# Performance work log

Measured on AMD Instinct MI355X. Metric: run time of the kernel, lower is better.

The kernel has to match this reference:

```python
import jax, jax.numpy as jnp
import numpy as np

B, A, L, D, IN = 4096, 11, 8, 256, 4
HID = 64  # mlp_dim in MS_HGNN modules
LINE = 64  # line_embedding output dim


def setup_inputs() -> dict:
    key = jax.random.key(0)
    ks = jax.random.split(key, 17)
    s = 0.02
    f = jnp.float32
    return {
        "inputs": jax.random.normal(ks[0], (B * A, L, IN), f),
        "W_in": jax.random.normal(ks[1], (IN, D), f) * s,
        "b_in": jnp.zeros((D,), f),
        "W_pos": jax.random.normal(ks[2], (2 * D, D), f) * s,
        "b_pos": jnp.zeros((D,), f),
        "W_fc2": jax.random.normal(ks[3], (L * D, D), f) * s,
        "b_fc2": jnp.zeros((D,), f),
        "W_fc3": jax.random.normal(ks[4], (D + A, D), f) * s,
        "b_fc3": jnp.zeros((D,), f),
        "Wh1": jax.random.normal(ks[5], (D, HID), f) * s,
        "We1": jax.random.normal(ks[6], (2 * HID, HID), f) * s,
        "Wn1": jax.random.normal(ks[7], (HID, D), f) * s,
        "Wh2": jax.random.normal(ks[8], (D, HID), f) * s,
        "We2": jax.random.normal(ks[9], (2 * HID, HID), f) * s,
        "Wn2": jax.random.normal(ks[10], (HID, D), f) * s,
        "W_line": jax.random.normal(ks[11], (D, LINE), f) * s,
        "batch_size": B,
        "agent_num": A,
    }


def _nmp(xf, Wh, We, Wn, w=None):
    # one round of neural message passing over the (hyper)graph of agents
    h = jax.nn.relu(xf @ Wh)  # [B, A, HID]
    b, a, hd = h.shape
    hi = jnp.broadcast_to(h[:, :, None, :], (b, a, a, hd))
    hj = jnp.broadcast_to(h[:, None, :, :], (b, a, a, hd))
    e = jax.nn.relu(jnp.concatenate([hi, hj], -1) @ We)  # [B, A, A, HID]
    if w is None:
        agg = e.mean(axis=2)
    else:
        agg = (w[..., None] * e).sum(axis=2) / (w.sum(axis=2)[..., None] + 1e-6)
    return agg @ Wn  # [B, A, D]


def reference(inputs, W_in, b_in, W_pos, b_pos, W_fc2, b_fc2, W_fc3, b_fc3,
              Wh1, We1, Wn1, Wh2, We2, Wn2, W_line, batch_size, agent_num):
    d = W_in.shape[1]
    length = inputs.shape[1]
    # input_fc
    tf_in = inputs @ W_in + b_in  # [B*A, L, D]
    # positional encoding (sin/cos interleaved), concat + fc (dropout in eval)
    pos = jnp.arange(length, dtype=tf_in.dtype)[:, None]
    div = jnp.exp(jnp.arange(0, d, 2, dtype=tf_in.dtype) * (-np.log(10000.0) / d))
    ang = pos * div  # [L, D/2]
    pe = jnp.stack([jnp.sin(ang), jnp.cos(ang)], -1).reshape(length, d)
    x = jnp.concatenate([tf_in, jnp.broadcast_to(pe, tf_in.shape)], -1) @ W_pos + b_pos
    # flatten time, input_fc2
    x = x.reshape(batch_size, agent_num, length * d)
    ftraj = x @ W_fc2 + b_fc2  # [B, A, D]
    # add_category (identity one-hot per agent) + input_fc3
    eye = jnp.broadcast_to(jnp.eye(agent_num, dtype=ftraj.dtype),
                           (batch_size, agent_num, agent_num))
    ftraj = jnp.concatenate([ftraj, eye], -1) @ W_fc3 + b_fc3
    # cosine-similarity correlation + per-scene adaptive thresholding
    q = ftraj / jnp.linalg.norm(ftraj, axis=2, keepdims=True)
    corr = jnp.einsum('bad,bcd->bac', q, q)
    a = corr.min(axis=(1, 2), keepdims=True)
    thr = jnp.where(a < 0.4, 0.4,
                    jnp.where((a > 0.4) & (a < 0.6), a + 0.1, a + 0.03))
    corr = jnp.where(corr < thr, jnp.zeros_like(corr), corr)
    adj = (corr > 0).astype(ftraj.dtype)  # binarized dynamic grouping mask
    # ordinary fully-connected interaction
    ftraj_inter = _nmp(ftraj, Wh1, We1, Wn1)
    # group-masked hyper interaction + line embedding
    hyp = _nmp(ftraj, Wh2, We2, Wn2, adj)
    feat_one = hyp @ W_line  # [B, A, LINE]
    out = jnp.concatenate([ftraj, ftraj_inter, feat_one], -1)
    return out.reshape(batch_size * agent_num, -1)
```

## Files before the change

kernel.cpp:

```cpp
#include <hip/hip_runtime.h>

#define TPB 256
#define TPM 192

constexpr int B_ = 4096, A_ = 11;
constexpr int R_ = B_ * A_;

constexpr int M_O     = 0;
constexpr int M2_O    = 8192;
constexpr int WC_O    = 16384;
constexpr int XB_O    = 17408;
constexpr int CB_O    = 19456;
constexpr int B2_O    = 19712;
constexpr int WN2L_O  = 22528;
constexpr int MH1_O   = 26624;
constexpr int BH1_O   = 28672;
constexpr int MH2_O   = 29376;
constexpr int BH2_O   = 31424;
constexpr int WFA1_O  = 32768;
constexpr int WFA2_O  = 49152;
constexpr int BEYE1_O = 65536;
constexpr int BEYE2_O = 66240;
constexpr int BB1_O   = 66944;
constexpr int BB2_O   = 67008;
constexpr int AG1_O   = 67584;
constexpr int SZ_RH   = R_ * 64;
constexpr int AG2_O   = AG1_O + SZ_RH;


__global__ __launch_bounds__(TPB) void k_preA(const float* __restrict__ Win,
                                              const float* __restrict__ bin,
                                              const float* __restrict__ Wpos,
                                              const float* __restrict__ bpos,
                                              const float* __restrict__ Wn2,
                                              const float* __restrict__ Wline,
                                              const float* __restrict__ Wfc3,
                                              const float* __restrict__ bfc3,
                                              const float* __restrict__ Wh1,
                                              const float* __restrict__ Wh2,
                                              float* __restrict__ ws) {
    __shared__ float red[8 * 33];
    const int t = threadIdx.x, o8 = t & 31, ks = t >> 5;
    const int bx = blockIdx.x;
    float p = 0.f;
    float base_add = 0.f;
    int out_idx = -1;
    if (bx < 64) {
        int o = bx * 32 + o8, l = o >> 8, j = o & 255;
        const float c0 = -logf(10000.f) / 256.f;
        for (int d = ks * 64; d < ks * 64 + 64; ++d) {
            float a;
            if (d < 256) a = bin[d];
            else {
                int dd = d - 256;
                float freq = expf((float)(dd & ~1) * c0);
                float ang = (float)l * freq;
                a = (dd & 1) ? cosf(ang) : sinf(ang);
            }
            p += a * Wpos[d * 256 + j];
        }
        out_idx = XB_O + o; base_add = bpos[j];
    } else if (bx < 192) {
        int o = (bx - 64) * 32 + o8, k = o >> 6, c = o & 63;
        #pragma unroll 8
        for (int d = ks * 32; d < ks * 32 + 32; ++d) p += Wn2[k * 256 + d] * Wline[d * 64 + c];
        out_idx = WN2L_O + o;
    } else if (bx < 704) {
        int o = (bx - 192) * 32 + o8, e = o >> 6, c = o & 63;
        #pragma unroll 8
        for (int d = ks * 32; d < ks * 32 + 32; ++d) p += Wfc3[e * 256 + d] * Wh1[d * 64 + c];
        out_idx = WFA1_O + o;
    } else if (bx < 1216) {
        int o = (bx - 704) * 32 + o8, e = o >> 6, c = o & 63;
        #pragma unroll 8
        for (int d = ks * 32; d < ks * 32 + 32; ++d) p += Wfc3[e * 256 + d] * Wh2[d * 64 + c];
        out_idx = WFA2_O + o;
    } else if (bx < 1238) {
        int o = (bx - 1216) * 32 + o8, a = o >> 6, c = o & 63;
        #pragma unroll 8
        for (int d = ks * 32; d < ks * 32 + 32; ++d) p += Wfc3[(256 + a) * 256 + d] * Wh1[d * 64 + c];
        out_idx = BEYE1_O + o;
    } else if (bx < 1260) {
        int o = (bx - 1238) * 32 + o8, a = o >> 6, c = o & 63;
        #pragma unroll 8
        for (int d = ks * 32; d < ks * 32 + 32; ++d) p += Wfc3[(256 + a) * 256 + d] * Wh2[d * 64 + c];
        out_idx = BEYE2_O + o;
    } else if (bx < 1262) {
        int c = (bx - 1260) * 32 + o8;
        #pragma unroll 8
        for (int d = ks * 32; d < ks * 32 + 32; ++d) p += bfc3[d] * Wh1[d * 64 + c];
        out_idx = BB1_O + c;
    } else if (bx < 1264) {
        int c = (bx - 1262) * 32 + o8;
        #pragma unroll 8
        for (int d = ks * 32; d < ks * 32 + 32; ++d) p += bfc3[d] * Wh2[d * 64 + c];
        out_idx = BB2_O + c;
    } else {
        int o = (bx - 1264) * 32 + o8, i = o >> 8, j = o & 255;
        #pragma unroll 8
        for (int d = ks * 32; d < ks * 32 + 32; ++d) p += Win[i * 256 + d] * Wpos[d * 256 + j];
        out_idx = WC_O + o;
    }
    red[ks * 33 + o8] = p;
    __shared__ float baseS[32];
    if (ks == 0) baseS[o8] = base_add;
    __syncthreads();
    if (t < 32) {
        float s = baseS[t];
        #pragma unroll
        for (int m = 0; m < 8; ++m) s += red[m * 33 + t];
        ws[out_idx - o8 + t] = s;
    }
}

__global__ __launch_bounds__(TPB) void k_preC(const float* __restrict__ Wfc2,
                                              const float* __restrict__ bfc2,
                                              float* __restrict__ ws) {
    __shared__ float red[8 * 33];
    const int t = threadIdx.x, o8 = t & 31, ks = t >> 5;
    const int bx = blockIdx.x;
    if (bx < 256) {
        int o = bx * 32 + o8, k = o >> 8, j = o & 255;
        int l = k >> 2, i = k & 3;
        const float* Ar = ws + WC_O + i * 256;
        const float* Br = Wfc2 + l * 65536 + j;
        float p = 0.f;
        #pragma unroll 8
        for (int d = ks * 32; d < ks * 32 + 32; ++d) p += Ar[d] * Br[d * 256];
        red[ks * 33 + o8] = p;
        __syncthreads();
        if (t < 32) {
            float s = 0.f;
            #pragma unroll
            for (int m = 0; m < 8; ++m) s += red[m * 33 + t];
            ws[M_O + bx * 32 + t] = s;
        }
    } else {
        int j = (bx - 256) * 32 + o8;
        const float* Ar = ws + XB_O;
        float p = 0.f;
        #pragma unroll 4
        for (int dk = ks * 256; dk < ks * 256 + 256; ++dk) p += Ar[dk] * Wfc2[dk * 256 + j];
        red[ks * 33 + o8] = p;
        __syncthreads();
        if (t < 32) {
            int jj = (bx - 256) * 32 + t;
            float s = bfc2[jj];
            #pragma unroll
            for (int m = 0; m < 8; ++m) s += red[m * 33 + t];
            ws[CB_O + jj] = s;
        }
    }
}

__global__ __launch_bounds__(TPB) void k_preD(const float* __restrict__ Wfc3,
                                              const float* __restrict__ bfc3,
                                              float* __restrict__ ws) {
    __shared__ float red[8 * 33];
    const int t = threadIdx.x, o8 = t & 31, ks = t >> 5;
    const int bx = blockIdx.x;
    float p = 0.f;
    int out_base = -1;
    int oo32 = 0;
    if (bx < 256) {
        int o = bx * 32 + o8, k = o >> 8, j = o & 255;
        const float* Ar = ws + M_O + k * 256;
        #pragma unroll 8
        for (int d = ks * 32; d < ks * 32 + 32; ++d) p += Ar[d] * Wfc3[d * 256 + j];
        out_base = M2_O; oo32 = bx * 32;
    } else if (bx < 344) {
        int o = (bx - 256) * 32 + o8, j = o & 255;
        const float* Ar = ws + CB_O;
        #pragma unroll 8
        for (int d = ks * 32; d < ks * 32 + 32; ++d) p += Ar[d] * Wfc3[d * 256 + j];
        out_base = B2_O; oo32 = (bx - 256) * 32;
    } else if (bx < 408) {
        int o = (bx - 344) * 32 + o8, k = o >> 6, c = o & 63;
        const float* Ar = ws + M_O + k * 256;
        const float* Br = ws + WFA1_O;
        #pragma unroll 8
        for (int d = ks * 32; d < ks * 32 + 32; ++d) p += Ar[d] * Br[d * 64 + c];
        out_base = MH1_O; oo32 = (bx - 344) * 32;
    } else if (bx < 472) {
        int o = (bx - 408) * 32 + o8, k = o >> 6, c = o & 63;
        const float* Ar = ws + M_O + k * 256;
        const float* Br = ws + WFA2_O;
        #pragma unroll 8
        for (int d = ks * 32; d < ks * 32 + 32; ++d) p += Ar[d] * Br[d * 64 + c];
        out_base = MH2_O; oo32 = (bx - 408) * 32;
    } else if (bx < 494) {
        int o = (bx - 472) * 32 + o8, c = o & 63;
        const float* Ar = ws + CB_O;
        const float* Br = ws + WFA1_O;
        #pragma unroll 8
        for (int d = ks * 32; d < ks * 32 + 32; ++d) p += Ar[d] * Br[d * 64 + c];
        out_base = BH1_O; oo32 = (bx - 472) * 32;
    } else {
        int o = (bx - 494) * 32 + o8, c = o & 63;
        const float* Ar = ws + CB_O;
        const float* Br = ws + WFA2_O;
        #pragma unroll 8
        for (int d = ks * 32; d < ks * 32 + 32; ++d) p += Ar[d] * Br[d * 64 + c];
        out_base = BH2_O; oo32 = (bx - 494) * 32;
    }
    red[ks * 33 + o8] = p;
    __syncthreads();
    if (t < 32) {
        int oo = oo32 + t;
        float s;
        if (out_base == B2_O) {
            int aa = oo >> 8, jj = oo & 255;
            s = bfc3[jj] + Wfc3[(256 + aa) * 256 + jj];
        } else if (out_base == BH1_O) {
            int aa = oo >> 6, cc = oo & 63;
            s = ws[BB1_O + cc] + ws[BEYE1_O + aa * 64 + cc];
        } else if (out_base == BH2_O) {
            int aa = oo >> 6, cc = oo & 63;
            s = ws[BB2_O + cc] + ws[BEYE2_O + aa * 64 + cc];
        } else s = 0.f;
        #pragma unroll
        for (int m = 0; m < 8; ++m) s += red[m * 33 + t];
        ws[out_base + oo] = s;
    }
}


__global__ __launch_bounds__(TPM) void k_main(const float* __restrict__ in,
                                              const float* __restrict__ We1g,
                                              const float* __restrict__ We2g,
                                              float* ws,
                                              float* out) {
    __shared__ float inS[22 * 36];
    __shared__ float buf[22 * 68];
    __shared__ float Bs[2048];
    __shared__ float dcS[242];
    __shared__ float thrS[2];
    const int t = threadIdx.x;
    const int rg = t >> 4, cg = t & 15;
    const int r0 = rg * 2, c0 = cg * 4;
    const int rowBlk = blockIdx.x * 22;
    const bool act = rg < 11;

    float4 pf0, pf1, pf2;
    auto pfLoad = [&](const float4* lo, const float4* hi) {
        pf0 = lo[t];
        pf1 = (t < 64) ? lo[t + 192] : hi[t - 64];
        if (t < 128) pf2 = hi[t + 128];
    };
    auto pfStore = [&]() {
        float4* d = (float4*)Bs;
        d[t] = pf0; d[t + 192] = pf1;
        if (t < 128) d[t + 384] = pf2;
    };

    pfLoad((const float4*)(ws + M2_O), (const float4*)(ws + M2_O) + 256);
    for (int o = t; o < 176; o += TPM) {
        int row = o >> 3, c4 = o & 7;
        *(float4*)&inS[row * 36 + c4 * 4] =
            *(const float4*)&in[(size_t)(rowBlk + row) * 32 + c4 * 4];
    }
    __syncthreads();

    float acc[2][16];
    #pragma unroll
    for (int r = 0; r < 2; ++r)
        #pragma unroll
        for (int c = 0; c < 16; ++c) acc[r][c] = 0.f;
    for (int kh = 0; kh < 4; ++kh) {
        pfStore();
        if (kh < 3) pfLoad((const float4*)(ws + M2_O) + (kh + 1) * 512,
                           (const float4*)(ws + M2_O) + (kh + 1) * 512 + 256);
        else        pfLoad((const float4*)(ws + MH1_O), (const float4*)(ws + MH1_O) + 256);
        __syncthreads();
        if (act) {
            #pragma unroll
            for (int kq = 0; kq < 2; ++kq) {
                float av[2][4];
                #pragma unroll
                for (int r = 0; r < 2; ++r) {
                    float4 a4 = *(const float4*)&inS[(r0 + r) * 36 + kh * 8 + kq * 4];
                    av[r][0] = a4.x; av[r][1] = a4.y; av[r][2] = a4.z; av[r][3] = a4.w;
                }
                #pragma unroll
                for (int kk = 0; kk < 4; ++kk) {
                    float4 b[4];
                    #pragma unroll
                    for (int j = 0; j < 4; ++j)
                        b[j] = *(const float4*)&Bs[(kq * 4 + kk) * 256 + c0 + j * 64];
                    #pragma unroll
                    for (int r = 0; r < 2; ++r) {
                        float a = av[r][kk];
                        #pragma unroll
                        for (int j = 0; j < 4; ++j) {
                            acc[r][j * 4 + 0] += a * b[j].x;
                            acc[r][j * 4 + 1] += a * b[j].y;
                            acc[r][j * 4 + 2] += a * b[j].z;
                            acc[r][j * 4 + 3] += a * b[j].w;
                        }
                    }
                }
            }
        }
        __syncthreads();
    }
    if (act) {
        #pragma unroll
        for (int r = 0; r < 2; ++r) {
            int row = r0 + r, il = row % 11;
            size_t ob = (size_t)(rowBlk + row) * 576;
            #pragma unroll
            for (int j = 0; j < 4; ++j) {
                float4 b2 = *(const float4*)&ws[B2_O + il * 256 + c0 + j * 64];
                acc[r][j * 4 + 0] += b2.x; acc[r][j * 4 + 1] += b2.y;
                acc[r][j * 4 + 2] += b2.z; acc[r][j * 4 + 3] += b2.w;
                *(float4*)&out[ob + c0 + j * 64] =
                    make_float4(acc[r][j * 4 + 0], acc[r][j * 4 + 1],
                                acc[r][j * 4 + 2], acc[r][j * 4 + 3]);
            }
        }
    }

    bool has0 = false;
    int s0_ = 0, i0_ = 0, j0_ = 0;
    if (t < 132) {
        has0 = true; s0_ = t / 66; int p = t % 66; int i = 0;
        while (p >= 11 - i) { p -= 11 - i; ++i; }
        i0_ = i; j0_ = i + p;
    }
    float dacc0 = 0.f;
    #pragma unroll
    for (int sl = 0; sl < 4; ++sl) {
        if (act) {
            #pragma unroll
            for (int r = 0; r < 2; ++r)
                *(float4*)&buf[(r0 + r) * 68 + c0] =
                    make_float4(acc[r][sl * 4 + 0], acc[r][sl * 4 + 1],
                                acc[r][sl * 4 + 2], acc[r][sl * 4 + 3]);
        }
        __syncthreads();
        if (has0) {
            const float* ra = &buf[(s0_ * 11 + i0_) * 68];
            const float* rb = &buf[(s0_ * 11 + j0_) * 68];
            #pragma unroll
            for (int c = 0; c < 16; ++c) {
                float4 a = *(const float4*)&ra[c * 4];
                float4 b = *(const float4*)&rb[c * 4];
                dacc0 += a.x * b.x + a.y * b.y + a.z * b.z + a.w * b.w;
            }
        }
        __syncthreads();
    }
    if (has0) { dcS[s0_ * 121 + i0_ * 11 + j0_] = dacc0;
                dcS[s0_ * 121 + j0_ * 11 + i0_] = dacc0; }
    __syncthreads();

    {
        float cc0, cc1 = 0.f;
        {
            int idx = t; int si = idx / 121, p = idx % 121, i = p / 11, j = p % 11;
            cc0 = dcS[idx] * rsqrtf(dcS[si * 121 + i * 12] * dcS[si * 121 + j * 12]);
        }
        if (t + TPM < 242) {
            int idx = t + TPM; int si = idx / 121, p = idx % 121, i = p / 11, j = p % 11;
            cc1 = dcS[idx] * rsqrtf(dcS[si * 121 + i * 12] * dcS[si * 121 + j * 12]);
        }
        __syncthreads();
        dcS[t] = cc0;
        if (t + TPM < 242) dcS[t + TPM] = cc1;
    }
    __syncthreads();
    if (t < 2) {
        float mn = 3.0e38f;
        for (int p = 0; p < 121; ++p) mn = fminf(mn, dcS[t * 121 + p]);
        thrS[t] = (mn < 0.4f) ? 0.4f : ((mn > 0.4f && mn < 0.6f) ? mn + 0.1f : mn + 0.03f);
    }
    __syncthreads();

    for (int st = 0; st < 2; ++st) {
        const float* bh = ws + (st ? BH2_O : BH1_O);
        const float* We = st ? We2g : We1g;
        pfStore();
        pfLoad((const float4*)(We), (const float4*)(We + 4096));
        __syncthreads();
        float hh[2][4];
        #pragma unroll
        for (int r = 0; r < 2; ++r)
            #pragma unroll
            for (int c = 0; c < 4; ++c) hh[r][c] = 0.f;
        if (act) {
            #pragma unroll
            for (int kq = 0; kq < 8; ++kq) {
                float av[2][4];
                #pragma unroll
                for (int r = 0; r < 2; ++r) {
                    float4 a4 = *(const float4*)&inS[(r0 + r) * 36 + kq * 4];
                    av[r][0] = a4.x; av[r][1] = a4.y; av[r][2] = a4.z; av[r][3] = a4.w;
                }
                #pragma unroll
                for (int kk = 0; kk < 4; ++kk) {
                    float4 b = *(const float4*)&Bs[(kq * 4 + kk) * 64 + c0];
                    #pragma unroll
                    for (int r = 0; r < 2; ++r) {
                        float a = av[r][kk];
                        hh[r][0] += a * b.x; hh[r][1] += a * b.y;
                        hh[r][2] += a * b.z; hh[r][3] += a * b.w;
                    }
                }
            }
            #pragma unroll
            for (int r = 0; r < 2; ++r) {
                int il = (r0 + r) % 11;
                float4 b = *(const float4*)&bh[il * 64 + c0];
                *(float4*)&buf[(r0 + r) * 68 + c0] =
                    make_float4(fmaxf(hh[r][0] + b.x, 0.f), fmaxf(hh[r][1] + b.y, 0.f),
                                fmaxf(hh[r][2] + b.z, 0.f), fmaxf(hh[r][3] + b.w, 0.f));
            }
        }
        __syncthreads();
        float uu[2][4], vv[2][4];
        #pragma unroll
        for (int r = 0; r < 2; ++r)
            #pragma unroll
            for (int c = 0; c < 4; ++c) { uu[r][c] = 0.f; vv[r][c] = 0.f; }
        for (int kh = 0; kh < 4; ++kh) {
            pfStore();
            if (kh < 3)
                pfLoad((const float4*)(We + (kh + 1) * 1024),
                       (const float4*)(We + 4096 + (kh + 1) * 1024));
            else if (st == 0)
                pfLoad((const float4*)(ws + MH2_O), (const float4*)(ws + MH2_O) + 256);
            __syncthreads();
            if (act) {
                #pragma unroll
                for (int kq = 0; kq < 4; ++kq) {
                    float av[2][4];
                    #pragma unroll
                    for (int r = 0; r < 2; ++r) {
                        float4 a4 = *(const float4*)&buf[(r0 + r) * 68 + kh * 16 + kq * 4];
                        av[r][0] = a4.x; av[r][1] = a4.y; av[r][2] = a4.z; av[r][3] = a4.w;
                    }
                    #pragma unroll
                    for (int kk = 0; kk < 4; ++kk) {
                        float4 bu = *(const float4*)&Bs[(kq * 4 + kk) * 64 + c0];
                        float4 bv = *(const float4*)&Bs[1024 + (kq * 4 + kk) * 64 + c0];
                        #pragma unroll
                        for (int r = 0; r < 2; ++r) {
                            float a = av[r][kk];
                            uu[r][0] += a * bu.x; uu[r][1] += a * bu.y;
                            uu[r][2] += a * bu.z; uu[r][3] += a * bu.w;
                            vv[r][0] += a * bv.x; vv[r][1] += a * bv.y;
                            vv[r][2] += a * bv.z; vv[r][3] += a * bv.w;
                        }
                    }
                }
            }
            __syncthreads();
        }
        if (act) {
            #pragma unroll
            for (int r = 0; r < 2; ++r)
                *(float4*)&buf[(r0 + r) * 68 + c0] =
                    make_float4(vv[r][0], vv[r][1], vv[r][2], vv[r][3]);
        }
        __syncthreads();
        if (act) {
            float* ag = ws + (st ? AG2_O : AG1_O);
            #pragma unroll
            for (int r = 0; r < 2; ++r) {
                int row = r0 + r, s = row / 11, il = row - s * 11;
                float th = thrS[s];
                float t0 = 0.f, t1 = 0.f, t2 = 0.f, t3 = 0.f, cnt = 0.f;
                #pragma unroll
                for (int j = 0; j < 11; ++j) {
                    float4 vj = *(const float4*)&buf[(s * 11 + j) * 68 + c0];
                    if (st == 0) {
                        t0 += fmaxf(uu[r][0] + vj.x, 0.f);
                        t1 += fmaxf(uu[r][1] + vj.y, 0.f);
                        t2 += fmaxf(uu[r][2] + vj.z, 0.f);
                        t3 += fmaxf(uu[r][3] + vj.w, 0.f);
                    } else {
                        float adj = (dcS[s * 121 + il * 11 + j] >= th) ? 1.f : 0.f;
                        t0 += adj * fmaxf(uu[r][0] + vj.x, 0.f);
                        t1 += adj * fmaxf(uu[r][1] + vj.y, 0.f);
                        t2 += adj * fmaxf(uu[r][2] + vj.z, 0.f);
                        t3 += adj * fmaxf(uu[r][3] + vj.w, 0.f);
                        cnt += adj;
                    }
                }
                float inv = (st == 0) ? (1.f / 11.f) : (1.f / (cnt + 1e-6f));
                *(float4*)&ag[(size_t)(rowBlk + row) * 64 + c0] =
                    make_float4(t0 * inv, t1 * inv, t2 * inv, t3 * inv);
            }
        }
        __syncthreads();
    }
}


__global__ __launch_bounds__(TPB) void k_tail(const float* __restrict__ Wn1,
                                              const float* __restrict__ ws,
                                              float* __restrict__ out) {
    __shared__ float aS[32 * 68];
    __shared__ float Bs[2048];
    const int t = threadIdx.x;
    const int rowBase = blockIdx.x * 32;
    const int tg = t >> 4, tc = t & 15;
    const int r0 = tg * 2, c0 = tc * 4;

    float4 pf0, pf1;
    auto pfLoad = [&](const float* src) {
        const float4* s = (const float4*)src;
        pf0 = s[t]; pf1 = s[t + 256];
    };
    auto pfStore = [&]() {
        float4* d = (float4*)Bs;
        d[t] = pf0; d[t + 256] = pf1;
    };

    pfLoad(Wn1);
    {
        const float4* s1 = (const float4*)(ws + AG1_O + (size_t)rowBase * 64);
        #pragma unroll
        for (int o = t; o < 512; o += TPB) {
            int row = o >> 4, c4 = o & 15;
            *(float4*)&aS[row * 68 + c4 * 4] = s1[o];
        }
    }

    float acc[2][16];
    #pragma unroll
    for (int r = 0; r < 2; ++r)
        #pragma unroll
        for (int c = 0; c < 16; ++c) acc[r][c] = 0.f;
    for (int kh = 0; kh < 8; ++kh) {
        pfStore();
        pfLoad(kh < 7 ? Wn1 + (kh + 1) * 2048 : ws + WN2L_O);
        __syncthreads();
        #pragma unroll
        for (int kq = 0; kq < 2; ++kq) {
            float av[2][4];
            #pragma unroll
            for (int r = 0; r < 2; ++r) {
                float4 a4 = *(const float4*)&aS[(r0 + r) * 68 + kh * 8 + kq * 4];
                av[r][0] = a4.x; av[r][1] = a4.y; av[r][2] = a4.z; av[r][3] = a4.w;
            }
            #pragma unroll
            for (int kk = 0; kk < 4; ++kk) {
                float4 b[4];
                #pragma unroll
                for (int j = 0; j < 4; ++j)
                    b[j] = *(const float4*)&Bs[(kq * 4 + kk) * 256 + c0 + j * 64];
                #pragma unroll
                for (int r = 0; r < 2; ++r) {
                    float a = av[r][kk];
                    #pragma unroll
                    for (int j = 0; j < 4; ++j) {
                        acc[r][j * 4 + 0] += a * b[j].x;
                        acc[r][j * 4 + 1] += a * b[j].y;
                        acc[r][j * 4 + 2] += a * b[j].z;
                        acc[r][j * 4 + 3] += a * b[j].w;
                    }
                }
            }
        }
        __syncthreads();
    }
    #pragma unroll
    for (int r = 0; r < 2; ++r) {
        size_t ob = (size_t)(rowBase + r0 + r) * 576 + 256;
        #pragma unroll
        for (int j = 0; j < 4; ++j)
            *(float4*)&out[ob + c0 + j * 64] =
                make_float4(acc[r][j * 4 + 0], acc[r][j * 4 + 1],
                            acc[r][j * 4 + 2], acc[r][j * 4 + 3]);
    }

    pfStore();
    pfLoad(ws + WN2L_O + 2048);
    {
        const float4* s2 = (const float4*)(ws + AG2_O + (size_t)rowBase * 64);
        #pragma unroll
        for (int o = t; o < 512; o += TPB) {
            int row = o >> 4, c4 = o & 15;
            *(float4*)&aS[row * 68 + c4 * 4] = s2[o];
        }
    }
    float fa[2][4];
    #pragma unroll
    for (int r = 0; r < 2; ++r)
        #pragma unroll
        for (int c = 0; c < 4; ++c) fa[r][c] = 0.f;
    for (int kh = 0; kh < 2; ++kh) {
        __syncthreads();
        if (kh == 1) { pfStore(); __syncthreads(); }
        #pragma unroll
        for (int kq = 0; kq < 8; ++kq) {
            float av[2][4];
            #pragma unroll
            for (int r = 0; r < 2; ++r) {
                float4 a4 = *(const float4*)&aS[(r0 + r) * 68 + kh * 32 + kq * 4];
                av[r][0] = a4.x; av[r][1] = a4.y; av[r][2] = a4.z; av[r][3] = a4.w;
            }
            #pragma unroll
            for (int kk = 0; kk < 4; ++kk) {
                float4 b = *(const float4*)&Bs[(kq * 4 + kk) * 64 + c0];
                #pragma unroll
                for (int r = 0; r < 2; ++r) {
                    float a = av[r][kk];
                    fa[r][0] += a * b.x; fa[r][1] += a * b.y;
                    fa[r][2] += a * b.z; fa[r][3] += a * b.w;
                }
            }
        }
    }
    #pragma unroll
    for (int r = 0; r < 2; ++r)
        *(float4*)&out[(size_t)(rowBase + r0 + r) * 576 + 512 + c0] =
            make_float4(fa[r][0], fa[r][1], fa[r][2], fa[r][3]);
}

extern "C" void kernel_launch(void* const* d_in, const int* in_sizes, int n_in,
                              void* d_out, int out_size, void* d_ws, size_t ws_size,
                              hipStream_t stream) {
    (void)in_sizes; (void)n_in; (void)out_size; (void)ws_size;
    const float* in     = (const float*)d_in[0];
    const float* W_in   = (const float*)d_in[1];
    const float* b_in   = (const float*)d_in[2];
    const float* W_pos  = (const float*)d_in[3];
    const float* b_pos  = (const float*)d_in[4];
    const float* W_fc2  = (const float*)d_in[5];
    const float* b_fc2  = (const float*)d_in[6];
    const float* W_fc3  = (const float*)d_in[7];
    const float* b_fc3  = (const float*)d_in[8];
    const float* Wh1    = (const float*)d_in[9];
    const float* We1    = (const float*)d_in[10];
    const float* Wn1    = (const float*)d_in[11];
    const float* Wh2    = (const float*)d_in[12];
    const float* We2    = (const float*)d_in[13];
    const float* Wn2    = (const float*)d_in[14];
    const float* W_line = (const float*)d_in[15];
    float* out = (float*)d_out;
    float* ws  = (float*)d_ws;

    k_preA<<<1296, TPB, 0, stream>>>(W_in, b_in, W_pos, b_pos, Wn2, W_line,
                                     W_fc3, b_fc3, Wh1, Wh2, ws);
    k_preC<<<264, TPB, 0, stream>>>(W_fc2, b_fc2, ws);
    k_preD<<<516, TPB, 0, stream>>>(W_fc3, b_fc3, ws);
    k_main<<<R_ / 22, TPM, 0, stream>>>(in, We1, We2, ws, out);
    k_tail<<<R_ / 32, TPB, 0, stream>>>(Wn1, ws, out);
}
```

Before: 154.8 us.

## Fuse tail projection GEMMs into main kernel, drop aggregate workspace round-trip

The separate k_tail kernel is removed. Its two projections (agg1 @ Wn1 into columns 256..511 and agg2 @ Wn2·W_line into columns 512..575) now run inside k_main, reading the aggregated messages from shared memory instead of writing them to workspace and reloading them. This removes one kernel launch and about 2×45K×64 floats of global write-plus-read traffic. In exchange, k_main gets more registers per thread and extra synchronisation phases, and only 176 of its 192 threads do useful work in the new GEMMs.

```diff
diff --git a/kernel.cpp b/kernel.cpp
--- a/kernel.cpp
+++ b/kernel.cpp
@@ -23,9 +23,6 @@
 constexpr int BEYE2_O = 66240;
 constexpr int BB1_O   = 66944;
 constexpr int BB2_O   = 67008;
-constexpr int AG1_O   = 67584;
-constexpr int SZ_RH   = R_ * 64;
-constexpr int AG2_O   = AG1_O + SZ_RH;
 
 
 __global__ __launch_bounds__(TPB) void k_preA(const float* __restrict__ Win,
@@ -228,8 +225,9 @@
 __global__ __launch_bounds__(TPM) void k_main(const float* __restrict__ in,
                                               const float* __restrict__ We1g,
                                               const float* __restrict__ We2g,
-                                              float* ws,
-                                              float* out) {
+                                              const float* __restrict__ Wn1,
+                                              const float* __restrict__ ws,
+                                              float* __restrict__ out) {
     __shared__ float inS[22 * 36];
     __shared__ float buf[22 * 68];
     __shared__ float Bs[2048];
@@ -428,7 +426,9 @@
                 pfLoad((const float4*)(We + (kh + 1) * 1024),
                        (const float4*)(We + 4096 + (kh + 1) * 1024));
             else if (st == 0)
-                pfLoad((const float4*)(ws + MH2_O), (const float4*)(ws + MH2_O) + 256);
+                pfLoad((const float4*)(Wn1), (const float4*)(Wn1) + 256);
+            else
+                pfLoad((const float4*)(ws + WN2L_O), (const float4*)(ws + WN2L_O) + 256);
             __syncthreads();
             if (act) {
                 #pragma unroll
@@ -463,8 +463,8 @@
                     make_float4(vv[r][0], vv[r][1], vv[r][2], vv[r][3]);
         }
         __syncthreads();
+        float ag[2][4];
         if (act) {
-            float* ag = ws + (st ? AG2_O : AG1_O);
             #pragma unroll
             for (int r = 0; r < 2; ++r) {
                 int row = r0 + r, s = row / 11, il = row - s * 11;
@@ -488,135 +488,115 @@
                     }
                 }
                 float inv = (st == 0) ? (1.f / 11.f) : (1.f / (cnt + 1e-6f));
-                *(float4*)&ag[(size_t)(rowBlk + row) * 64 + c0] =
-                    make_float4(t0 * inv, t1 * inv, t2 * inv, t3 * inv);
-            }
-        }
-        __syncthreads();
-    }
-}
-
-
-__global__ __launch_bounds__(TPB) void k_tail(const float* __restrict__ Wn1,
-                                              const float* __restrict__ ws,
-                                              float* __restrict__ out) {
-    __shared__ float aS[32 * 68];
-    __shared__ float Bs[2048];
-    const int t = threadIdx.x;
-    const int rowBase = blockIdx.x * 32;
-    const int tg = t >> 4, tc = t & 15;
-    const int r0 = tg * 2, c0 = tc * 4;
-
-    float4 pf0, pf1;
-    auto pfLoad = [&](const float* src) {
-        const float4* s = (const float4*)src;
-        pf0 = s[t]; pf1 = s[t + 256];
-    };
-    auto pfStore = [&]() {
-        float4* d = (float4*)Bs;
-        d[t] = pf0; d[t + 256] = pf1;
-    };
-
-    pfLoad(Wn1);
-    {
-        const float4* s1 = (const float4*)(ws + AG1_O + (size_t)rowBase * 64);
-        #pragma unroll
-        for (int o = t; o < 512; o += TPB) {
-            int row = o >> 4, c4 = o & 15;
-            *(float4*)&aS[row * 68 + c4 * 4] = s1[o];
-        }
-    }
-
-    float acc[2][16];
-    #pragma unroll
-    for (int r = 0; r < 2; ++r)
-        #pragma unroll
-        for (int c = 0; c < 16; ++c) acc[r][c] = 0.f;
-    for (int kh = 0; kh < 8; ++kh) {
-        pfStore();
-        pfLoad(kh < 7 ? Wn1 + (kh + 1) * 2048 : ws + WN2L_O);
-        __syncthreads();
-        #pragma unroll
-        for (int kq = 0; kq < 2; ++kq) {
-            float av[2][4];
-            #pragma unroll
-            for (int r = 0; r < 2; ++r) {
-                float4 a4 = *(const float4*)&aS[(r0 + r) * 68 + kh * 8 + kq * 4];
-                av[r][0] = a4.x; av[r][1] = a4.y; av[r][2] = a4.z; av[r][3] = a4.w;
-            }
-            #pragma unroll
-            for (int kk = 0; kk < 4; ++kk) {
-                float4 b[4];
-                #pragma unroll
-                for (int j = 0; j < 4; ++j)
-                    b[j] = *(const float4*)&Bs[(kq * 4 + kk) * 256 + c0 + j * 64];
+                ag[r][0] = t0 * inv; ag[r][1] = t1 * inv;
+                ag[r][2] = t2 * inv; ag[r][3] = t3 * inv;
+            }
+        }
+        __syncthreads();
+        if (act) {
+            #pragma unroll
+            for (int r = 0; r < 2; ++r)
+                *(float4*)&buf[(r0 + r) * 68 + c0] =
+                    make_float4(ag[r][0], ag[r][1], ag[r][2], ag[r][3]);
+        }
+        __syncthreads();
+
+        if (st == 0) {
+            float ac2[2][16];
+            #pragma unroll
+            for (int r = 0; r < 2; ++r)
+                #pragma unroll
+                for (int c = 0; c < 16; ++c) ac2[r][c] = 0.f;
+            for (int kh = 0; kh < 8; ++kh) {
+                pfStore();
+                if (kh < 7) pfLoad((const float4*)(Wn1) + (kh + 1) * 512,
+                                   (const float4*)(Wn1) + (kh + 1) * 512 + 256);
+                else        pfLoad((const float4*)(ws + MH2_O), (const float4*)(ws + MH2_O) + 256);
+                __syncthreads();
+                if (act) {
+                    #pragma unroll
+                    for (int kq = 0; kq < 2; ++kq) {
+                        float av[2][4];
+                        #pragma unroll
+                        for (int r = 0; r < 2; ++r) {
+                            float4 a4 = *(const float4*)&buf[(r0 + r) * 68 + kh * 8 + kq * 4];
+                            av[r][0] = a4.x; av[r][1] = a4.y; av[r][2] = a4.z; av[r][3] = a4.w;
+                        }
+                        #pragma unroll
+                        for (int kk = 0; kk < 4; ++kk) {
+                            float4 b[4];
+                            #pragma unroll
+                            for (int j = 0; j < 4; ++j)
+                                b[j] = *(const float4*)&Bs[(kq * 4 + kk) * 256 + c0 + j * 64];
+                            #pragma unroll
+                            for (int r = 0; r < 2; ++r) {
+                                float a = av[r][kk];
+                                #pragma unroll
+                                for (int j = 0; j < 4; ++j) {
+                                    ac2[r][j * 4 + 0] += a * b[j].x;
+                                    ac2[r][j * 4 + 1] += a * b[j].y;
+                                    ac2[r][j * 4 + 2] += a * b[j].z;
+                                    ac2[r][j * 4 + 3] += a * b[j].w;
+                                }
+                            }
+                        }
+                    }
+                }
+                __syncthreads();
+            }
+            if (act) {
                 #pragma unroll
                 for (int r = 0; r < 2; ++r) {
-                    float a = av[r][kk];
-                    #pragma unroll
-                    for (int j = 0; j < 4; ++j) {
-                        acc[r][j * 4 + 0] += a * b[j].x;
-                        acc[r][j * 4 + 1] += a * b[j].y;
-                        acc[r][j * 4 + 2] += a * b[j].z;
-                        acc[r][j * 4 + 3] += a * b[j].w;
+                    size_t ob = (size_t)(rowBlk + r0 + r) * 576 + 256;
+                    #pragma unroll
+                    for (int j = 0; j < 4; ++j)
+                        *(float4*)&out[ob + c0 + j * 64] =
+                            make_float4(ac2[r][j * 4 + 0], ac2[r][j * 4 + 1],
+                                        ac2[r][j * 4 + 2], ac2[r][j * 4 + 3]);
+                }
+            }
+        } else {
+            float fa[2][4];
+            #pragma unroll
+            for (int r = 0; r < 2; ++r)
+                #pragma unroll
+                for (int c = 0; c < 4; ++c) fa[r][c] = 0.f;
+            for (int kh = 0; kh < 2; ++kh) {
+                pfStore();
+                if (kh == 0) pfLoad((const float4*)(ws + WN2L_O) + 512,
+                                    (const float4*)(ws + WN2L_O) + 768);
+                __syncthreads();
+                if (act) {
+                    #pragma unroll
+                    for (int kq = 0; kq < 8; ++kq) {
+                        float av[2][4];
+                        #pragma unroll
+                        for (int r = 0; r < 2; ++r) {
+                            float4 a4 = *(const float4*)&buf[(r0 + r) * 68 + kh * 32 + kq * 4];
+                            av[r][0] = a4.x; av[r][1] = a4.y; av[r][2] = a4.z; av[r][3] = a4.w;
+                        }
+                        #pragma unroll
+                        for (int kk = 0; kk < 4; ++kk) {
+                            float4 b = *(const float4*)&Bs[(kq * 4 + kk) * 64 + c0];
+                            #pragma unroll
+                            for (int r = 0; r < 2; ++r) {
+                                float a = av[r][kk];
+                                fa[r][0] += a * b.x; fa[r][1] += a * b.y;
+                                fa[r][2] += a * b.z; fa[r][3] += a * b.w;
+                            }
+                        }
                     }
                 }
-            }
-        }
-        __syncthreads();
-    }
-    #pragma unroll
-    for (int r = 0; r < 2; ++r) {
-        size_t ob = (size_t)(rowBase + r0 + r) * 576 + 256;
-        #pragma unroll
-        for (int j = 0; j < 4; ++j)
-            *(float4*)&out[ob + c0 + j * 64] =
-                make_float4(acc[r][j * 4 + 0], acc[r][j * 4 + 1],
-                            acc[r][j * 4 + 2], acc[r][j * 4 + 3]);
-    }
-
-    pfStore();
-    pfLoad(ws + WN2L_O + 2048);
-    {
-        const float4* s2 = (const float4*)(ws + AG2_O + (size_t)rowBase * 64);
-        #pragma unroll
-        for (int o = t; o < 512; o += TPB) {
-            int row = o >> 4, c4 = o & 15;
-            *(float4*)&aS[row * 68 + c4 * 4] = s2[o];
-        }
-    }
-    float fa[2][4];
-    #pragma unroll
-    for (int r = 0; r < 2; ++r)
-        #pragma unroll
-        for (int c = 0; c < 4; ++c) fa[r][c] = 0.f;
-    for (int kh = 0; kh < 2; ++kh) {
-        __syncthreads();
-        if (kh == 1) { pfStore(); __syncthreads(); }
-        #pragma unroll
-        for (int kq = 0; kq < 8; ++kq) {
-            float av[2][4];
-            #pragma unroll
-            for (int r = 0; r < 2; ++r) {
-                float4 a4 = *(const float4*)&aS[(r0 + r) * 68 + kh * 32 + kq * 4];
-                av[r][0] = a4.x; av[r][1] = a4.y; av[r][2] = a4.z; av[r][3] = a4.w;
-            }
-            #pragma unroll
-            for (int kk = 0; kk < 4; ++kk) {
-                float4 b = *(const float4*)&Bs[(kq * 4 + kk) * 64 + c0];
-                #pragma unroll
-                for (int r = 0; r < 2; ++r) {
-                    float a = av[r][kk];
-                    fa[r][0] += a * b.x; fa[r][1] += a * b.y;
-                    fa[r][2] += a * b.z; fa[r][3] += a * b.w;
-                }
-            }
-        }
-    }
-    #pragma unroll
-    for (int r = 0; r < 2; ++r)
-        *(float4*)&out[(size_t)(rowBase + r0 + r) * 576 + 512 + c0] =
-            make_float4(fa[r][0], fa[r][1], fa[r][2], fa[r][3]);
+                if (kh == 0) __syncthreads();
+            }
+            if (act) {
+                #pragma unroll
+                for (int r = 0; r < 2; ++r)
+                    *(float4*)&out[(size_t)(rowBlk + r0 + r) * 576 + 512 + c0] =
+                        make_float4(fa[r][0], fa[r][1], fa[r][2], fa[r][3]);
+            }
+        }
+    }
 }
 
 extern "C" void kernel_launch(void* const* d_in, const int* in_sizes, int n_in,
@@ -646,6 +626,5 @@
                                      W_fc3, b_fc3, Wh1, Wh2, ws);
     k_preC<<<264, TPB, 0, stream>>>(W_fc2, b_fc2, ws);
     k_preD<<<516, TPB, 0, stream>>>(W_fc3, b_fc3, ws);
-    k_main<<<R_ / 22, TPM, 0, stream>>>(in, We1, We2, ws, out);
-    k_tail<<<R_ / 32, TPB, 0, stream>>>(Wn1, ws, out);
+    k_main<<<R_ / 22, TPM, 0, stream>>>(in, We1, We2, Wn1, ws, out);
 }
```

New measurement: 186.1 us. +20.2%, slower.

## Process one scene per block in k_main instead of two

Applied to the files above, without the earlier changes.

k_main now handles a single scene (11 agent rows) per block with one row per thread group, and launches 4096 blocks instead of 2048. Per-thread register tiles shrink from 2 rows to 1, shared-memory footprint drops, and the correlation/threshold logic is simplified to one scene. This trades register-level reuse of each shared-memory weight load (now used for one row instead of two) for more blocks, lower register pressure and higher occupancy. Weight staging is also repeated across twice as many blocks, which adds global and shared traffic.

```diff
diff --git a/kernel.cpp b/kernel.cpp
--- a/kernel.cpp
+++ b/kernel.cpp
@@ -230,15 +230,16 @@
                                               const float* __restrict__ We2g,
                                               float* ws,
                                               float* out) {
-    __shared__ float inS[22 * 36];
-    __shared__ float buf[22 * 68];
+    __shared__ float inS[11 * 36];
+    __shared__ float buf[11 * 68];
     __shared__ float Bs[2048];
-    __shared__ float dcS[242];
-    __shared__ float thrS[2];
+    __shared__ float dcS[121];
+    __shared__ float thrS1;
     const int t = threadIdx.x;
     const int rg = t >> 4, cg = t & 15;
-    const int r0 = rg * 2, c0 = cg * 4;
-    const int rowBlk = blockIdx.x * 22;
+    const int c0 = cg * 4;
+    const int row = rg;
+    const int rowBlk = blockIdx.x * 11;
     const bool act = rg < 11;
 
     float4 pf0, pf1, pf2;
@@ -254,18 +255,16 @@
     };
 
     pfLoad((const float4*)(ws + M2_O), (const float4*)(ws + M2_O) + 256);
-    for (int o = t; o < 176; o += TPM) {
-        int row = o >> 3, c4 = o & 7;
-        *(float4*)&inS[row * 36 + c4 * 4] =
-            *(const float4*)&in[(size_t)(rowBlk + row) * 32 + c4 * 4];
+    if (t < 88) {
+        int r = t >> 3, c4 = t & 7;
+        *(float4*)&inS[r * 36 + c4 * 4] =
+            *(const float4*)&in[(size_t)(rowBlk + r) * 32 + c4 * 4];
     }
     __syncthreads();
 
-    float acc[2][16];
+    float acc[16];
     #pragma unroll
-    for (int r = 0; r < 2; ++r)
-        #pragma unroll
-        for (int c = 0; c < 16; ++c) acc[r][c] = 0.f;
+    for (int c = 0; c < 16; ++c) acc[c] = 0.f;
     for (int kh = 0; kh < 4; ++kh) {
         pfStore();
         if (kh < 3) pfLoad((const float4*)(ws + M2_O) + (kh + 1) * 512,
@@ -275,28 +274,21 @@
         if (act) {
             #pragma unroll
             for (int kq = 0; kq < 2; ++kq) {
-                float av[2][4];
-                #pragma unroll
-                for (int r = 0; r < 2; ++r) {
-                    float4 a4 = *(const float4*)&inS[(r0 + r) * 36 + kh * 8 + kq * 4];
-                    av[r][0] = a4.x; av[r][1] = a4.y; av[r][2] = a4.z; av[r][3] = a4.w;
-                }
+                float4 a4 = *(const float4*)&inS[row * 36 + kh * 8 + kq * 4];
+                float av[4] = {a4.x, a4.y, a4.z, a4.w};
                 #pragma unroll
                 for (int kk = 0; kk < 4; ++kk) {
                     float4 b[4];
                     #pragma unroll
                     for (int j = 0; j < 4; ++j)
                         b[j] = *(const float4*)&Bs[(kq * 4 + kk) * 256 + c0 + j * 64];
+                    float a = av[kk];
                     #pragma unroll
-                    for (int r = 0; r < 2; ++r) {
-                        float a = av[r][kk];
-                        #pragma unroll
-                        for (int j = 0; j < 4; ++j) {
-                            acc[r][j * 4 + 0] += a * b[j].x;
-                            acc[r][j * 4 + 1] += a * b[j].y;
-                            acc[r][j * 4 + 2] += a * b[j].z;
-                            acc[r][j * 4 + 3] += a * b[j].w;
-                        }
+                    for (int j = 0; j < 4; ++j) {
+                        acc[j * 4 + 0] += a * b[j].x;
+                        acc[j * 4 + 1] += a * b[j].y;
+                        acc[j * 4 + 2] += a * b[j].z;
+                        acc[j * 4 + 3] += a * b[j].w;
                     }
                 }
             }
@@ -304,43 +296,36 @@
         __syncthreads();
     }
     if (act) {
-        #pragma unroll
-        for (int r = 0; r < 2; ++r) {
-            int row = r0 + r, il = row % 11;
-            size_t ob = (size_t)(rowBlk + row) * 576;
-            #pragma unroll
-            for (int j = 0; j < 4; ++j) {
-                float4 b2 = *(const float4*)&ws[B2_O + il * 256 + c0 + j * 64];
-                acc[r][j * 4 + 0] += b2.x; acc[r][j * 4 + 1] += b2.y;
-                acc[r][j * 4 + 2] += b2.z; acc[r][j * 4 + 3] += b2.w;
-                *(float4*)&out[ob + c0 + j * 64] =
-                    make_float4(acc[r][j * 4 + 0], acc[r][j * 4 + 1],
-                                acc[r][j * 4 + 2], acc[r][j * 4 + 3]);
-            }
+        size_t ob = (size_t)(rowBlk + row) * 576;
+        #pragma unroll
+        for (int j = 0; j < 4; ++j) {
+            float4 b2 = *(const float4*)&ws[B2_O + row * 256 + c0 + j * 64];
+            acc[j * 4 + 0] += b2.x; acc[j * 4 + 1] += b2.y;
+            acc[j * 4 + 2] += b2.z; acc[j * 4 + 3] += b2.w;
+            *(float4*)&out[ob + c0 + j * 64] =
+                make_float4(acc[j * 4 + 0], acc[j * 4 + 1],
+                            acc[j * 4 + 2], acc[j * 4 + 3]);
         }
     }
 
     bool has0 = false;
-    int s0_ = 0, i0_ = 0, j0_ = 0;
-    if (t < 132) {
-        has0 = true; s0_ = t / 66; int p = t % 66; int i = 0;
+    int i0_ = 0, j0_ = 0;
+    if (t < 66) {
+        has0 = true; int p = t; int i = 0;
         while (p >= 11 - i) { p -= 11 - i; ++i; }
         i0_ = i; j0_ = i + p;
     }
     float dacc0 = 0.f;
     #pragma unroll
     for (int sl = 0; sl < 4; ++sl) {
-        if (act) {
-            #pragma unroll
-            for (int r = 0; r < 2; ++r)
-                *(float4*)&buf[(r0 + r) * 68 + c0] =
-                    make_float4(acc[r][sl * 4 + 0], acc[r][sl * 4 + 1],
-                                acc[r][sl * 4 + 2], acc[r][sl * 4 + 3]);
-        }
+        if (act)
+            *(float4*)&buf[row * 68 + c0] =
+                make_float4(acc[sl * 4 + 0], acc[sl * 4 + 1],
+                            acc[sl * 4 + 2], acc[sl * 4 + 3]);
         __syncthreads();
         if (has0) {
-            const float* ra = &buf[(s0_ * 11 + i0_) * 68];
-            const float* rb = &buf[(s0_ * 11 + j0_) * 68];
+            const float* ra = &buf[i0_ * 68];
+            const float* rb = &buf[j0_ * 68];
             #pragma unroll
             for (int c = 0; c < 16; ++c) {
                 float4 a = *(const float4*)&ra[c * 4];
@@ -350,29 +335,24 @@
         }
         __syncthreads();
     }
-    if (has0) { dcS[s0_ * 121 + i0_ * 11 + j0_] = dacc0;
-                dcS[s0_ * 121 + j0_ * 11 + i0_] = dacc0; }
+    if (has0) { dcS[i0_ * 11 + j0_] = dacc0;
+                dcS[j0_ * 11 + i0_] = dacc0; }
     __syncthreads();
 
     {
-        float cc0, cc1 = 0.f;
-        {
-            int idx = t; int si = idx / 121, p = idx % 121, i = p / 11, j = p % 11;
-            cc0 = dcS[idx] * rsqrtf(dcS[si * 121 + i * 12] * dcS[si * 121 + j * 12]);
-        }
-        if (t + TPM < 242) {
-            int idx = t + TPM; int si = idx / 121, p = idx % 121, i = p / 11, j = p % 11;
-            cc1 = dcS[idx] * rsqrtf(dcS[si * 121 + i * 12] * dcS[si * 121 + j * 12]);
-        }
-        __syncthreads();
-        dcS[t] = cc0;
-        if (t + TPM < 242) dcS[t + TPM] = cc1;
+        float cc0 = 0.f;
+        if (t < 121) {
+            int i = t / 11, j = t % 11;
+            cc0 = dcS[t] * rsqrtf(dcS[i * 12] * dcS[j * 12]);
+        }
+        __syncthreads();
+        if (t < 121) dcS[t] = cc0;
     }
     __syncthreads();
-    if (t < 2) {
+    if (t == 0) {
         float mn = 3.0e38f;
-        for (int p = 0; p < 121; ++p) mn = fminf(mn, dcS[t * 121 + p]);
-        thrS[t] = (mn < 0.4f) ? 0.4f : ((mn > 0.4f && mn < 0.6f) ? mn + 0.1f : mn + 0.03f);
+        for (int p = 0; p < 121; ++p) mn = fminf(mn, dcS[p]);
+        thrS1 = (mn < 0.4f) ? 0.4f : ((mn > 0.4f && mn < 0.6f) ? mn + 0.1f : mn + 0.03f);
     }
     __syncthreads();
 
@@ -382,46 +362,27 @@
         pfStore();
         pfLoad((const float4*)(We), (const float4*)(We + 4096));
         __syncthreads();
-        float hh[2][4];
-        #pragma unroll
-        for (int r = 0; r < 2; ++r)
-            #pragma unroll
-            for (int c = 0; c < 4; ++c) hh[r][c] = 0.f;
+        float hh[4] = {0.f, 0.f, 0.f, 0.f};
         if (act) {
             #pragma unroll
             for (int kq = 0; kq < 8; ++kq) {
-                float av[2][4];
-                #pragma unroll
-                for (int r = 0; r < 2; ++r) {
-                    float4 a4 = *(const float4*)&inS[(r0 + r) * 36 + kq * 4];
-                    av[r][0] = a4.x; av[r][1] = a4.y; av[r][2] = a4.z; av[r][3] = a4.w;
-                }
+                float4 a4 = *(const float4*)&inS[row * 36 + kq * 4];
+                float av[4] = {a4.x, a4.y, a4.z, a4.w};
                 #pragma unroll
                 for (int kk = 0; kk < 4; ++kk) {
                     float4 b = *(const float4*)&Bs[(kq * 4 + kk) * 64 + c0];
-                    #pragma unroll
-                    for (int r = 0; r < 2; ++r) {
-                        float a = av[r][kk];
-                        hh[r][0] += a * b.x; hh[r][1] += a * b.y;
-                        hh[r][2] += a * b.z; hh[r][3] += a * b.w;
-                    }
+                    float a = av[kk];
+                    hh[0] += a * b.x; hh[1] += a * b.y;
+                    hh[2] += a * b.z; hh[3] += a * b.w;
                 }
             }
-            #pragma unroll
-            for (int r = 0; r < 2; ++r) {
-                int il = (r0 + r) % 11;
-                float4 b = *(const float4*)&bh[il * 64 + c0];
-                *(float4*)&buf[(r0 + r) * 68 + c0] =
-                    make_float4(fmaxf(hh[r][0] + b.x, 0.f), fmaxf(hh[r][1] + b.y, 0.f),
-                                fmaxf(hh[r][2] + b.z, 0.f), fmaxf(hh[r][3] + b.w, 0.f));
-            }
-        }
-        __syncthreads();
-        float uu[2][4], vv[2][4];
-        #pragma unroll
-        for (int r = 0; r < 2; ++r)
-            #pragma unroll
-            for (int c = 0; c < 4; ++c) { uu[r][c] = 0.f; vv[r][c] = 0.f; }
+            float4 b = *(const float4*)&bh[row * 64 + c0];
+            *(float4*)&buf[row * 68 + c0] =
+                make_float4(fmaxf(hh[0] + b.x, 0.f), fmaxf(hh[1] + b.y, 0.f),
+                            fmaxf(hh[2] + b.z, 0.f), fmaxf(hh[3] + b.w, 0.f));
+        }
+        __syncthreads();
+        float uu[4] = {0.f, 0.f, 0.f, 0.f}, vv[4] = {0.f, 0.f, 0.f, 0.f};
         for (int kh = 0; kh < 4; ++kh) {
             pfStore();
             if (kh < 3)
@@ -433,64 +394,49 @@
             if (act) {
                 #pragma unroll
                 for (int kq = 0; kq < 4; ++kq) {
-                    float av[2][4];
-                    #pragma unroll
-                    for (int r = 0; r < 2; ++r) {
-                        float4 a4 = *(const float4*)&buf[(r0 + r) * 68 + kh * 16 + kq * 4];
-                        av[r][0] = a4.x; av[r][1] = a4.y; av[r][2] = a4.z; av[r][3] = a4.w;
-                    }
+                    float4 a4 = *(const float4*)&buf[row * 68 + kh * 16 + kq * 4];
+                    float av[4] = {a4.x, a4.y, a4.z, a4.w};
                     #pragma unroll
                     for (int kk = 0; kk < 4; ++kk) {
                         float4 bu = *(const float4*)&Bs[(kq * 4 + kk) * 64 + c0];
                         float4 bv = *(const float4*)&Bs[1024 + (kq * 4 + kk) * 64 + c0];
-                        #pragma unroll
-                        for (int r = 0; r < 2; ++r) {
-                            float a = av[r][kk];
-                            uu[r][0] += a * bu.x; uu[r][1] += a * bu.y;
-                            uu[r][2] += a * bu.z; uu[r][3] += a * bu.w;
-                            vv[r][0] += a * bv.x; vv[r][1] += a * bv.y;
-                            vv[r][2] += a * bv.z; vv[r][3] += a * bv.w;
-                        }
+                        float a = av[kk];
+                        uu[0] += a * bu.x; uu[1] += a * bu.y;
+                        uu[2] += a * bu.z; uu[3] += a * bu.w;
+                        vv[0] += a * bv.x; vv[1] += a * bv.y;
+                        vv[2] += a * bv.z; vv[3] += a * bv.w;
                     }
                 }
             }
             __syncthreads();
         }
-        if (act) {
-            #pragma unroll
-            for (int r = 0; r < 2; ++r)
-                *(float4*)&buf[(r0 + r) * 68 + c0] =
-                    make_float4(vv[r][0], vv[r][1], vv[r][2], vv[r][3]);
-        }
+        if (act)
+            *(float4*)&buf[row * 68 + c0] = make_float4(vv[0], vv[1], vv[2], vv[3]);
         __syncthreads();
         if (act) {
             float* ag = ws + (st ? AG2_O : AG1_O);
-            #pragma unroll
-            for (int r = 0; r < 2; ++r) {
-                int row = r0 + r, s = row / 11, il = row - s * 11;
-                float th = thrS[s];
-                float t0 = 0.f, t1 = 0.f, t2 = 0.f, t3 = 0.f, cnt = 0.f;
-                #pragma unroll
-                for (int j = 0; j < 11; ++j) {
-                    float4 vj = *(const float4*)&buf[(s * 11 + j) * 68 + c0];
-                    if (st == 0) {
-                        t0 += fmaxf(uu[r][0] + vj.x, 0.f);
-                        t1 += fmaxf(uu[r][1] + vj.y, 0.f);
-                        t2 += fmaxf(uu[r][2] + vj.z, 0.f);
-                        t3 += fmaxf(uu[r][3] + vj.w, 0.f);
-                    } else {
-                        float adj = (dcS[s * 121 + il * 11 + j] >= th) ? 1.f : 0.f;
-                        t0 += adj * fmaxf(uu[r][0] + vj.x, 0.f);
-                        t1 += adj * fmaxf(uu[r][1] + vj.y, 0.f);
-                        t2 += adj * fmaxf(uu[r][2] + vj.z, 0.f);
-                        t3 += adj * fmaxf(uu[r][3] + vj.w, 0.f);
-                        cnt += adj;
-                    }
+            float th = thrS1;
+            float t0 = 0.f, t1 = 0.f, t2 = 0.f, t3 = 0.f, cnt = 0.f;
+            #pragma unroll
+            for (int j = 0; j < 11; ++j) {
+                float4 vj = *(const float4*)&buf[j * 68 + c0];
+                if (st == 0) {
+                    t0 += fmaxf(uu[0] + vj.x, 0.f);
+                    t1 += fmaxf(uu[1] + vj.y, 0.f);
+                    t2 += fmaxf(uu[2] + vj.z, 0.f);
+                    t3 += fmaxf(uu[3] + vj.w, 0.f);
+                } else {
+                    float adj = (dcS[row * 11 + j] >= th) ? 1.f : 0.f;
+                    t0 += adj * fmaxf(uu[0] + vj.x, 0.f);
+                    t1 += adj * fmaxf(uu[1] + vj.y, 0.f);
+                    t2 += adj * fmaxf(uu[2] + vj.z, 0.f);
+                    t3 += adj * fmaxf(uu[3] + vj.w, 0.f);
+                    cnt += adj;
                 }
-                float inv = (st == 0) ? (1.f / 11.f) : (1.f / (cnt + 1e-6f));
-                *(float4*)&ag[(size_t)(rowBlk + row) * 64 + c0] =
-                    make_float4(t0 * inv, t1 * inv, t2 * inv, t3 * inv);
-            }
+            }
+            float inv = (st == 0) ? (1.f / 11.f) : (1.f / (cnt + 1e-6f));
+            *(float4*)&ag[(size_t)(rowBlk + row) * 64 + c0] =
+                make_float4(t0 * inv, t1 * inv, t2 * inv, t3 * inv);
         }
         __syncthreads();
     }
@@ -646,6 +592,6 @@
                                      W_fc3, b_fc3, Wh1, Wh2, ws);
     k_preC<<<264, TPB, 0, stream>>>(W_fc2, b_fc2, ws);
     k_preD<<<516, TPB, 0, stream>>>(W_fc3, b_fc3, ws);
-    k_main<<<R_ / 22, TPM, 0, stream>>>(in, We1, We2, ws, out);
+    k_main<<<B_, TPM, 0, stream>>>(in, We1, We2, ws, out);
     k_tail<<<R_ / 32, TPB, 0, stream>>>(Wn1, ws, out);
 }
```

Measured after the change: 168.3 us. 8.7% more time.
